# Kernel tuning notes

Measured on AMD Instinct MI355X. Metric: run time of the kernel, lower is better.

The kernel has to match this reference:

```python
import jax, jax.numpy as jnp
import numpy as np

T, B, L, CTX, H = 512, 512, 16, 64, 128
STATE_DIM, SHOT, PID, DATA = 32, 12, 35, 23


def setup_inputs() -> dict:
    key = jax.random.key(0)
    ks = jax.random.split(key, 64)
    k = iter(ks)
    def rn(shape, s=0.1):
        return (jax.random.normal(next(k), shape) * s).astype(jnp.float32)
    xs = jax.random.normal(next(k), (T, B, DATA), jnp.float32)
    xs = xs.at[:, :, 12].set(jax.random.randint(next(k), (T, B), 0, SHOT).astype(jnp.float32))
    xs = xs.at[:, :, 17].set(jax.random.randint(next(k), (T, B), 0, PID).astype(jnp.float32))
    xs = xs.at[:, :, 20].set(jax.random.randint(next(k), (T, B), 0, SHOT).astype(jnp.float32))
    return dict(
        total_xs=jnp.zeros((1,), jnp.float32),
        xs=xs,
        ts=jnp.linspace(0.0, 2.0, T).astype(jnp.float32),
        noise_std=jnp.asarray(0.1, jnp.float32),
        z0_noise=jax.random.normal(next(k), (B, L), jnp.float32),
        bm_noise=jax.random.normal(next(k), (T - 1, B, L), jnp.float32),
        shot_emb=rn((SHOT, 8)), player_emb=rn((PID, 8)),
        gru_wih=rn((3 * H, STATE_DIM)), gru_whh=rn((3 * H, H)),
        gru_bih=rn((3 * H,)), gru_bhh=rn((3 * H,)),
        enc_w=rn((CTX, H)), enc_b=rn((CTX,)),
        qz0_w=rn((2 * L, CTX)), qz0_b=rn((2 * L,)),
        f_w1=rn((H, L + CTX)), f_b1=rn((H,)), f_w2=rn((H, H)), f_b2=rn((H,)),
        f_w3=rn((L, H)), f_b3=rn((L,)),
        h_w1=rn((H, L)), h_b1=rn((H,)), h_w2=rn((H, H)), h_b2=rn((H,)),
        h_w3=rn((L, H)), h_b3=rn((L,)),
        g_w1=rn((L, H)), g_b1=rn((L, H)), g_w2=rn((L, H)), g_b2=rn((L,)),
        proj_w=rn((STATE_DIM, L)), proj_b=rn((STATE_DIM,)),
        pz0_mean=jnp.zeros((1, L), jnp.float32), pz0_logstd=jnp.zeros((1, L), jnp.float32),
        act_w=rn((128, L)), act_b=rn((128,)),
        act_land_w=rn((2, 128)), act_shot_w=rn((SHOT, 128)), act_move_w=rn((2, 128)),
    )


def _forward(xs, noise_std, shot_emb, player_emb, gru_wih, gru_whh, gru_bih, gru_bhh,
             enc_w, enc_b, qz0_w, qz0_b,
             f_w1, f_b1, f_w2, f_b2, f_w3, f_b3,
             h_w1, h_b1, h_w2, h_b2, h_w3, h_b3,
             g_w1, g_b1, g_w2, g_b2,
             proj_w, proj_b, pz0_mean, pz0_logstd,
             act_w, act_b, act_land_w, act_shot_w, act_move_w,
             ts, z0_noise, bm_noise):
    # --- SDE_embed_and_transform: replace shot/player id cols with embeddings ---
    state = xs[:, :, :18]
    shot_ids = state[:, :, 12].astype(jnp.int32)
    pid_ids = state[:, :, 17].astype(jnp.int32)
    state_t = jnp.concatenate([state[:, :, :12], shot_emb[shot_ids],
                               state[:, :, 13:17], player_emb[pid_ids]], axis=-1)  # (T,B,32)
    xs_t = jnp.concatenate([state_t, xs[:, :, 18:]], axis=-1)  # (T,B,37)
    # --- Encoder: GRU over time-reversed states, linear head, flip back ---
    def gru_step(h, xt):
        gi = xt @ gru_wih.T + gru_bih
        gh = h @ gru_whh.T + gru_bhh
        ir, iz, inn = jnp.split(gi, 3, axis=-1)
        hr, hz, hn = jnp.split(gh, 3, axis=-1)
        r = jax.nn.sigmoid(ir + hr)
        zg = jax.nn.sigmoid(iz + hz)
        n = jnp.tanh(inn + r * hn)
        hnew = (1.0 - zg) * n + zg * h
        return hnew, hnew
    h0 = jnp.zeros((xs.shape[1], gru_whh.shape[1]), xs.dtype)
    _, hs = jax.lax.scan(gru_step, h0, state_t[::-1])
    ctx = (hs @ enc_w.T + enc_b)[::-1]  # (T,B,CTX)
    # --- posterior z0 ---
    qm, qls = jnp.split(ctx[0] @ qz0_w.T + qz0_b, 2, axis=1)
    z0 = qm + jnp.exp(qls) * z0_noise
    # --- Euler-Maruyama with logqp; searchsorted(right) -> ctx[min(i+1,T-1)] = ctx[i+1] ---
    dts = ts[1:] - ts[:-1]  # (T-1,)
    dW = jnp.sqrt(dts)[:, None, None] * bm_noise
    ctx_steps = ctx[1:]
    def mlp3(x, w1, b1, w2, b2, w3, b3):
        h1 = jax.nn.softplus(x @ w1.T + b1)
        h2 = jax.nn.softplus(h1 @ w2.T + b2)
        return h2 @ w3.T + b3
    def g_diag(y):  # (B,L): per-latent-dim scalar nets, batched over L
        hg = jax.nn.softplus(y[:, :, None] * g_w1[None] + g_b1[None])  # (B,L,H)
        return jax.nn.sigmoid(jnp.einsum('blh,lh->bl', hg, g_w2) + g_b2)
    def sde_step(z, inp):
        c, dw, dt = inp
        f_val = mlp3(jnp.concatenate([z, c], axis=1), f_w1, f_b1, f_w2, f_b2, f_w3, f_b3)
        h_val = mlp3(z, h_w1, h_b1, h_w2, h_b2, h_w3, h_b3)
        g_val = g_diag(z)
        u = (f_val - h_val) / g_val
        logr = 0.5 * jnp.sum(u * u, axis=1) * dt
        z_new = z + f_val * dt + g_val * dw
        return z_new, (z_new, logr)
    _, (z_tail, log_ratio) = jax.lax.scan(sde_step, z0, (ctx_steps, dW, dts))
    zs = jnp.concatenate([z0[None], z_tail], axis=0)  # (T,B,L)
    _xs = zs @ proj_w.T + proj_b  # (T,B,32)
    # --- action model losses ---
    a = jax.nn.relu(zs @ act_w.T + act_b)
    land = (a @ act_land_w.T).reshape(-1, 2)
    shot_logits = (a @ act_shot_w.T).reshape(-1, act_shot_w.shape[0])
    move = (a @ act_move_w.T).reshape(-1, 2)
    true_actions = xs_t[:, :, -5:]
    true_land = true_actions[:, :, :2].reshape(-1, 2)
    true_move = true_actions[:, :, 3:].reshape(-1, 2)
    true_shot = true_actions[:, :, 2].astype(jnp.int32).reshape(-1)
    land_loss = jnp.mean((land - true_land) ** 2)
    move_loss = jnp.mean((move - true_move) ** 2)
    logp = jax.nn.log_softmax(shot_logits, axis=-1)
    picked = jnp.take_along_axis(logp, true_shot[:, None], axis=1)[:, 0]
    mask = (true_shot != 0).astype(logp.dtype)  # CrossEntropy ignore_index=0
    shot_loss = -jnp.sum(picked * mask) / jnp.maximum(jnp.sum(mask), 1.0)
    # --- reconstruction log-likelihood ---
    xs_state = xs_t[:, :, :STATE_DIM]
    LOG2PI = 1.8378770664093453
    log_pxs = jnp.mean(jnp.sum(
        -0.5 * ((xs_state - _xs) / noise_std) ** 2 - jnp.log(noise_std) - 0.5 * LOG2PI,
        axis=(0, 2)))
    # --- KL(q(z0) || p(z0)) ---
    var_q = jnp.exp(2.0 * qls)
    var_p = jnp.exp(2.0 * pz0_logstd)
    kl = pz0_logstd - qls + (var_q + (qm - pz0_mean) ** 2) / (2.0 * var_p) - 0.5
    logqp0 = jnp.mean(jnp.sum(kl, axis=1))
    logqp_path = jnp.mean(jnp.sum(log_ratio, axis=0))
    return log_pxs, logqp0 + logqp_path + land_loss + shot_loss + move_loss


def reference(total_xs, xs, ts, noise_std, z0_noise, bm_noise, shot_emb, player_emb,
              gru_wih, gru_whh, gru_bih, gru_bhh, enc_w, enc_b, qz0_w, qz0_b,
              f_w1, f_b1, f_w2, f_b2, f_w3, f_b3, h_w1, h_b1, h_w2, h_b2, h_w3, h_b3,
              g_w1, g_b1, g_w2, g_b2, proj_w, proj_b, pz0_mean, pz0_logstd,
              act_w, act_b, act_land_w, act_shot_w, act_move_w):
    return _forward(xs, noise_std, shot_emb, player_emb, gru_wih, gru_whh, gru_bih, gru_bhh,
                    enc_w, enc_b, qz0_w, qz0_b,
                    f_w1, f_b1, f_w2, f_b2, f_w3, f_b3,
                    h_w1, h_b1, h_w2, h_b2, h_w3, h_b3,
                    g_w1, g_b1, g_w2, g_b2,
                    proj_w, proj_b, pz0_mean, pz0_logstd,
                    act_w, act_b, act_land_w, act_shot_w, act_move_w,
                    ts, z0_noise, bm_noise)
```

## Files before the change

### kernel.cpp

```cpp
#include <hip/hip_runtime.h>
#include <cstdint>

typedef _Float16 f16;
typedef _Float16 f16x2 __attribute__((ext_vector_type(2)));

#define T_STEPS 512
#define B_SZ 512
#define LOG2PI 1.8378770664093453f

__device__ __forceinline__ void barrier_lds() {
  asm volatile("s_waitcnt lgkmcnt(0)" ::: "memory");
  __builtin_amdgcn_s_barrier();
  asm volatile("" ::: "memory");
}

__device__ __forceinline__ uint32_t packh2(float a, float b) {
  f16x2 v; v[0] = (f16)a; v[1] = (f16)b;
  return __builtin_bit_cast(uint32_t, v);
}

__device__ __forceinline__ float fdot2(uint32_t a, uint32_t b, float c) {
#if defined(__AMDGCN__) && __has_builtin(__builtin_amdgcn_fdot2)
  return __builtin_amdgcn_fdot2(__builtin_bit_cast(f16x2, a),
                                __builtin_bit_cast(f16x2, b), c, false);
#else
  f16x2 x = __builtin_bit_cast(f16x2, a), y = __builtin_bit_cast(f16x2, b);
  return c + (float)x[0] * (float)y[0] + (float)x[1] * (float)y[1];
#endif
}

#define DOT4(acc, w0, w1, w2, w3, v)                                     \
  do {                                                                   \
    acc = fdot2((w0), (v).x, acc); acc = fdot2((w1), (v).y, acc);        \
    acc = fdot2((w2), (v).z, acc); acc = fdot2((w3), (v).w, acc);        \
  } while (0)

__device__ __forceinline__ float sigmoidf_(float x) {
  return 1.0f / (1.0f + __expf(-x));
}
__device__ __forceinline__ float tanhf_(float x) {
  float ax = fabsf(x);
  float t = __expf(-2.0f * ax);
  float r = (1.0f - t) / (1.0f + t);
  return copysignf(r, x);
}
__device__ __forceinline__ float softplusf_(float x) {
  return fmaxf(x, 0.0f) + __logf(1.0f + __expf(-fabsf(x)));
}

__global__ __launch_bounds__(256) void k_embed(
    const float* __restrict__ xs, const float* __restrict__ shot_emb,
    const float* __restrict__ player_emb, f16* __restrict__ state_t,
    float* __restrict__ accums) {
  if (blockIdx.x == 0 && threadIdx.x < 16) accums[threadIdx.x] = 0.0f;
  size_t idx = (size_t)blockIdx.x * 256 + threadIdx.x;
  const float* xp = xs + idx * 23;
  f16* op = state_t + idx * 32;
  int sid = (int)xp[12];
  int pid = (int)xp[17];
#pragma unroll
  for (int i = 0; i < 12; ++i) op[i] = (f16)xp[i];
  const float* se = shot_emb + sid * 8;
#pragma unroll
  for (int i = 0; i < 8; ++i) op[12 + i] = (f16)se[i];
#pragma unroll
  for (int i = 0; i < 4; ++i) op[20 + i] = (f16)xp[13 + i];
  const float* pe = player_emb + pid * 8;
#pragma unroll
  for (int i = 0; i < 8; ++i) op[24 + i] = (f16)pe[i];
}

__global__ __launch_bounds__(256) void k_gtab(
    const float* __restrict__ gw1, const float* __restrict__ gb1,
    const float* __restrict__ gw2, const float* __restrict__ gb2,
    float* __restrict__ g_tab) {
  int gid = blockIdx.x * 256 + threadIdx.x;
  int l = gid >> 16, yi = gid & 0xffff;
  f16 hy = __builtin_bit_cast(f16, (unsigned short)yi);
  float y = (float)hy;
  const float* w1 = gw1 + l * 128;
  const float* b1 = gb1 + l * 128;
  const float* w2 = gw2 + l * 128;
  float a0 = 0.f, a1 = 0.f;
#pragma unroll 8
  for (int h = 0; h < 128; h += 2) {
    a0 = fmaf(softplusf_(fmaf(y, w1[h], b1[h])), w2[h], a0);
    a1 = fmaf(softplusf_(fmaf(y, w1[h + 1], b1[h + 1])), w2[h + 1], a1);
  }
  g_tab[gid] = sigmoidf_(a0 + a1 + gb2[l]);
}

__global__ __launch_bounds__(256, 2) void k_gru(
    const f16* __restrict__ state_t, const float* __restrict__ wih,
    const float* __restrict__ whh, const float* __restrict__ bih,
    const float* __restrict__ bhh, const float* __restrict__ enc_w,
    const float* __restrict__ enc_b, const float* __restrict__ qz0_w,
    const float* __restrict__ qz0_b, const float* __restrict__ z0_noise,
    const float* __restrict__ pz0_mean, const float* __restrict__ pz0_logstd,
    f16* __restrict__ ctx, float* __restrict__ z0_out,
    float* __restrict__ accums) {
  __shared__ uint32_t s_x[16];
  __shared__ uint32_t s_h[64];
  __shared__ float s_gates[128 * 4];
  __shared__ float s_encp[64 * 2];
  __shared__ float s_ctx0[64];
  __shared__ float s_q[32];

  const int tid = threadIdx.x;
  const int bg = blockIdx.x;
  const int r = tid >> 1, hh = tid & 1;
  const int ec = r & 63, eks = r >> 6;
  const uint32_t* stu = (const uint32_t*)state_t;

  uint32_t wR[32], wZ[32], wN[32];
  uint32_t wRx[8], wZx[8], wNx[8];
  uint32_t wE[16];
  {
    const float* w0 = whh + (size_t)(0 * 128 + r) * 128 + hh * 64;
    const float* w1 = whh + (size_t)(1 * 128 + r) * 128 + hh * 64;
    const float* w2 = whh + (size_t)(2 * 128 + r) * 128 + hh * 64;
#pragma unroll
    for (int i = 0; i < 32; ++i) {
      wR[i] = packh2(w0[2 * i], w0[2 * i + 1]);
      wZ[i] = packh2(w1[2 * i], w1[2 * i + 1]);
      wN[i] = packh2(w2[2 * i], w2[2 * i + 1]);
    }
    const float* x0 = wih + (size_t)(0 * 128 + r) * 32 + hh * 16;
    const float* x1 = wih + (size_t)(1 * 128 + r) * 32 + hh * 16;
    const float* x2 = wih + (size_t)(2 * 128 + r) * 32 + hh * 16;
#pragma unroll
    for (int i = 0; i < 8; ++i) {
      wRx[i] = packh2(x0[2 * i], x0[2 * i + 1]);
      wZx[i] = packh2(x1[2 * i], x1[2 * i + 1]);
      wNx[i] = packh2(x2[2 * i], x2[2 * i + 1]);
    }
    const float* we = enc_w + (size_t)ec * 128 + eks * 64 + hh * 32;
#pragma unroll
    for (int i = 0; i < 16; ++i) wE[i] = packh2(we[2 * i], we[2 * i + 1]);
  }
  const float bR = bih[r] + bhh[r];
  const float bZ = bih[128 + r] + bhh[128 + r];
  const float bNi = bih[256 + r];
  const float bNh = bhh[256 + r];
  float encbr = 0.f;
  if (tid >= 128 && tid < 192) encbr = enc_b[tid - 128];

  float h_old = 0.0f;
  if (tid < 64) s_h[tid] = 0u;
  if (tid < 4)
    *(uint4*)&s_x[tid * 4] =
        *(const uint4*)(stu + ((size_t)(T_STEPS - 1) * B_SZ + bg) * 16 + tid * 4);
  __syncthreads();

  for (int t = T_STEPS - 1; t >= 0; --t) {
    uint4 xpref = make_uint4(0, 0, 0, 0);
    if (tid >= 252 && t > 0)
      xpref = *(const uint4*)(stu +
                              ((size_t)(t - 1) * B_SZ + bg) * 16 + (tid - 252) * 4);
    {
      const uint4* xq = (const uint4*)&s_x[hh * 8];
      uint4 xv0 = xq[0], xv1 = xq[1];
      const uint4* hq = (const uint4*)&s_h[hh * 32];
      float aR = 0.f, aZ = 0.f, aNi = 0.f, aNh = 0.f;
      DOT4(aR, wRx[0], wRx[1], wRx[2], wRx[3], xv0);
      DOT4(aR, wRx[4], wRx[5], wRx[6], wRx[7], xv1);
      DOT4(aZ, wZx[0], wZx[1], wZx[2], wZx[3], xv0);
      DOT4(aZ, wZx[4], wZx[5], wZx[6], wZx[7], xv1);
      DOT4(aNi, wNx[0], wNx[1], wNx[2], wNx[3], xv0);
      DOT4(aNi, wNx[4], wNx[5], wNx[6], wNx[7], xv1);
#pragma unroll
      for (int j = 0; j < 8; ++j) {
        uint4 hv = hq[j];
        DOT4(aR, wR[4 * j], wR[4 * j + 1], wR[4 * j + 2], wR[4 * j + 3], hv);
        DOT4(aZ, wZ[4 * j], wZ[4 * j + 1], wZ[4 * j + 2], wZ[4 * j + 3], hv);
        DOT4(aNh, wN[4 * j], wN[4 * j + 1], wN[4 * j + 2], wN[4 * j + 3], hv);
      }
      aR += __shfl_xor(aR, 1);
      aZ += __shfl_xor(aZ, 1);
      aNi += __shfl_xor(aNi, 1);
      aNh += __shfl_xor(aNh, 1);
      if (hh == 0) {
        s_gates[r * 4 + 0] = aR + bR;
        s_gates[r * 4 + 2] = aNi + bNi;
      } else {
        s_gates[r * 4 + 1] = aZ + bZ;
        s_gates[r * 4 + 3] = aNh + bNh;
      }
      if (t < T_STEPS - 1) {
        const uint4* eq = (const uint4*)&s_h[eks * 32 + hh * 16];
        float aE = 0.f;
#pragma unroll
        for (int j = 0; j < 4; ++j) {
          uint4 ev = eq[j];
          DOT4(aE, wE[4 * j], wE[4 * j + 1], wE[4 * j + 2], wE[4 * j + 3], ev);
        }
        aE += __shfl_xor(aE, 1);
        if (hh == 0) s_encp[ec * 2 + eks] = aE;
      }
    }
    barrier_lds();
    if (tid < 128) {
      const float4 gt = *(const float4*)&s_gates[tid * 4];
      float rr = sigmoidf_(gt.x), zg = sigmoidf_(gt.y);
      float n = tanhf_(gt.z + rr * gt.w);
      float hnew = (1.0f - zg) * n + zg * h_old;
      h_old = hnew;
      ((f16*)&s_h[0])[tid] = (f16)hnew;
    } else if (tid < 192) {
      int c = tid - 128;
      if (t < T_STEPS - 1) {
        float v = s_encp[c * 2] + s_encp[c * 2 + 1] + encbr;
        ctx[((size_t)(t + 1) * B_SZ + bg) * 64 + c] = (f16)v;
      }
    }
    if (tid >= 252 && t > 0) *(uint4*)&s_x[(tid - 252) * 4] = xpref;
    barrier_lds();
  }

  {
    const uint4* eq = (const uint4*)&s_h[eks * 32 + hh * 16];
    float aE = 0.f;
#pragma unroll
    for (int j = 0; j < 4; ++j) {
      uint4 ev = eq[j];
      DOT4(aE, wE[4 * j], wE[4 * j + 1], wE[4 * j + 2], wE[4 * j + 3], ev);
    }
    aE += __shfl_xor(aE, 1);
    if (hh == 0) s_encp[ec * 2 + eks] = aE;
  }
  __syncthreads();
  if (tid < 64) {
    float v = s_encp[tid * 2] + s_encp[tid * 2 + 1] + enc_b[tid];
    ctx[(size_t)bg * 64 + tid] = (f16)v;
    s_ctx0[tid] = v;
  }
  __syncthreads();
  if (tid < 32) {
    float acc = qz0_b[tid];
#pragma unroll 8
    for (int k = 0; k < 64; ++k) acc += qz0_w[tid * 64 + k] * s_ctx0[k];
    s_q[tid] = acc;
  }
  __syncthreads();
  if (tid < 16) {
    float qm = s_q[tid], qls = s_q[16 + tid];
    float z0v = qm + __expf(qls) * z0_noise[bg * 16 + tid];
    z0_out[bg * 16 + tid] = z0v;
    float pm = pz0_mean[tid], pls = pz0_logstd[tid];
    float var_q = __expf(2.0f * qls);
    float var_p = __expf(2.0f * pls);
    float dm = qm - pm;
    float kl = pls - qls + (var_q + dm * dm) / (2.0f * var_p) - 0.5f;
    atomicAdd(&accums[5], kl);
  }
}

__global__ __launch_bounds__(256, 2) void k_sde(
    const f16* __restrict__ ctx, const float* __restrict__ z0_in,
    const float* __restrict__ ts, const float* __restrict__ bm_noise,
    const float* __restrict__ fw1, const float* __restrict__ fb1,
    const float* __restrict__ fw2, const float* __restrict__ fb2,
    const float* __restrict__ fw3, const float* __restrict__ fb3,
    const float* __restrict__ hw1, const float* __restrict__ hb1,
    const float* __restrict__ hw2, const float* __restrict__ hb2,
    const float* __restrict__ hw3, const float* __restrict__ hb3,
    const float* __restrict__ g_tab,
    f16* __restrict__ zs, float* __restrict__ accums) {
  __shared__ uint32_t s_x2[40];
  __shared__ uint32_t s_h1[2][64];
  __shared__ uint32_t s_h2[2][64];
  __shared__ float s_dts[T_STEPS];

  const int tid = threadIdx.x;
  const int bg = blockIdx.x;
  const uint4* ctx4 = (const uint4*)ctx;

  const int r1 = tid >> 1, hh = tid & 1;
  const int mlp2 = tid >> 7, u2 = tid & 127;
  const int l3 = (tid >> 3) & 15;
  const int mlp3 = (tid >> 2) & 1;
  const int kq = tid & 3;
  const bool p3act = (tid < 128);
  const bool zlane = p3act && ((tid & 7) == 0);
  const bool stg = (tid >= 128 && tid < 136);

  uint32_t uw1f[20], uw1h[4], wP2[64], wP3[16];
  float bf1r, bh1r, bias2r, fb3r = 0.f, hb3r = 0.f;
  {
    const float* w = fw1 + (size_t)r1 * 80 + hh * 40;
#pragma unroll
    for (int i = 0; i < 20; ++i) uw1f[i] = packh2(w[2 * i], w[2 * i + 1]);
    bf1r = fb1[r1];
  }
  {
    const float* w = hw1 + (size_t)r1 * 16 + hh * 8;
#pragma unroll
    for (int i = 0; i < 4; ++i) uw1h[i] = packh2(w[2 * i], w[2 * i + 1]);
    bh1r = hb1[r1];
  }
  {
    const float* w = (mlp2 ? hw2 : fw2) + (size_t)u2 * 128;
#pragma unroll
    for (int i = 0; i < 64; ++i) wP2[i] = packh2(w[2 * i], w[2 * i + 1]);
    bias2r = (mlp2 ? hb2 : fb2)[u2];
  }
  if (p3act) {
    const float* w = (mlp3 ? hw3 : fw3) + (size_t)l3 * 128 + kq * 32;
#pragma unroll
    for (int i = 0; i < 16; ++i) wP3[i] = packh2(w[2 * i], w[2 * i + 1]);
    fb3r = fb3[l3];
    hb3r = hb3[l3];
  }
  for (int i = tid; i < T_STEPS - 1; i += 256) s_dts[i] = ts[i + 1] - ts[i];

  float zreg = 0.f, bmc = 0.f, path_acc = 0.f;
  uint4 cpref = make_uint4(0, 0, 0, 0);
  if (zlane) {
    zreg = z0_in[bg * 16 + l3];
    ((f16*)&s_x2[0])[l3] = (f16)zreg;
    zs[(size_t)bg * 16 + l3] = (f16)zreg;
    bmc = bm_noise[(size_t)bg * 16 + l3];
  }
  if (stg) {
    int q = tid - 128;
    uint4 v = ctx4[((size_t)1 * B_SZ + bg) * 8 + q];
    *(uint4*)&s_x2[8 + q * 4] = v;
  }
  __syncthreads();

  for (int t = 0; t < T_STEPS - 1; ++t) {
    float bmn = 0.f, gvp = 0.f;
    if (zlane) {
      unsigned short zb = __builtin_bit_cast(unsigned short, (f16)zreg);
      gvp = g_tab[l3 * 65536 + (int)zb];
      if (t < T_STEPS - 2)
        bmn = bm_noise[((size_t)(t + 1) * B_SZ + bg) * 16 + l3];
    }
    if (stg && t <= T_STEPS - 3)
      cpref = ctx4[((size_t)(t + 2) * B_SZ + bg) * 8 + (tid - 128)];

    {
      const uint4* xq = (const uint4*)&s_x2[0];
      const int base = hh * 5;
      float a0 = 0.f, a1 = 0.f;
      {
        uint4 v0 = xq[base + 0], v1 = xq[base + 1];
        DOT4(a0, uw1f[0], uw1f[1], uw1f[2], uw1f[3], v0);
        DOT4(a1, uw1f[4], uw1f[5], uw1f[6], uw1f[7], v1);
        uint4 v2 = xq[base + 2], v3 = xq[base + 3];
        DOT4(a0, uw1f[8], uw1f[9], uw1f[10], uw1f[11], v2);
        DOT4(a1, uw1f[12], uw1f[13], uw1f[14], uw1f[15], v3);
        uint4 v4 = xq[base + 4];
        DOT4(a0, uw1f[16], uw1f[17], uw1f[18], uw1f[19], v4);
      }
      float af = a0 + a1;
      uint4 vz = xq[hh];
      float ah = 0.f;
      DOT4(ah, uw1h[0], uw1h[1], uw1h[2], uw1h[3], vz);
      float ff = af + __shfl_xor(af, 1);
      float fh = ah + __shfl_xor(ah, 1);
      if (hh == 0)
        ((f16*)&s_h1[0][0])[r1] = (f16)softplusf_(ff + bf1r);
      else
        ((f16*)&s_h1[1][0])[r1] = (f16)softplusf_(fh + bh1r);
    }
    barrier_lds();
    {
      const uint4* hq = (const uint4*)&s_h1[mlp2][0];
      float a0 = 0.f, a1 = 0.f;
#pragma unroll
      for (int j = 0; j < 16; j += 2) {
        uint4 v0 = hq[j], v1 = hq[j + 1];
        DOT4(a0, wP2[4 * j], wP2[4 * j + 1], wP2[4 * j + 2], wP2[4 * j + 3], v0);
        DOT4(a1, wP2[4 * j + 4], wP2[4 * j + 5], wP2[4 * j + 6], wP2[4 * j + 7], v1);
      }
      ((f16*)&s_h2[mlp2][0])[u2] = (f16)softplusf_(a0 + a1 + bias2r);
    }
    barrier_lds();
    if (p3act) {
      const uint4* hq = (const uint4*)&s_h2[mlp3][kq * 16];
      float a0 = 0.f, a1 = 0.f;
#pragma unroll
      for (int j = 0; j < 4; j += 2) {
        uint4 v0 = hq[j], v1 = hq[j + 1];
        DOT4(a0, wP3[4 * j], wP3[4 * j + 1], wP3[4 * j + 2], wP3[4 * j + 3], v0);
        DOT4(a1, wP3[4 * j + 4], wP3[4 * j + 5], wP3[4 * j + 6], wP3[4 * j + 7], v1);
      }
      float a = a0 + a1;
      float s1 = a + __shfl_xor(a, 1);
      float s2 = s1 + __shfl_xor(s1, 2);
      float other = __shfl_xor(s2, 4);
      if ((tid & 7) == 0) {
        float fv = s2 + fb3r;
        float hv = other + hb3r;
        float gv = gvp;
        float dt = s_dts[t];
        float u_ = (fv - hv) / gv;
        float ls = u_ * u_;
        ls += __shfl_xor(ls, 8);
        ls += __shfl_xor(ls, 16);
        ls += __shfl_xor(ls, 32);
        if ((tid & 63) == 0) path_acc += 0.5f * ls * dt;
        float dw = sqrtf(dt) * bmc;
        float zn = zreg + fv * dt + gv * dw;
        zreg = zn;
        ((f16*)&s_x2[0])[l3] = (f16)zn;
        zs[((size_t)(t + 1) * B_SZ + bg) * 16 + l3] = (f16)zn;
        bmc = bmn;
      }
    } else if (stg && t <= T_STEPS - 3) {
      *(uint4*)&s_x2[8 + (tid - 128) * 4] = cpref;
    }
    barrier_lds();
  }
  if (tid == 0 || tid == 64) atomicAdd(&accums[6], path_acc);
}

__global__ __launch_bounds__(256) void k_dec(
    const f16* __restrict__ zs, const f16* __restrict__ state_t,
    const float* __restrict__ xs, const float* __restrict__ proj_w,
    const float* __restrict__ proj_b, const float* __restrict__ act_w,
    const float* __restrict__ act_b, const float* __restrict__ land_w,
    const float* __restrict__ shot_w, const float* __restrict__ move_w,
    float* __restrict__ accums) {
  __shared__ uint32_t s_proj[8 * 32];
  __shared__ uint32_t s_act[8 * 128];
  __shared__ uint32_t s_head[128 * 8];
  __shared__ float s_pb[32], s_ab[128];
  __shared__ float s_red[4 * 5];

  const int tid = threadIdx.x;
  for (int id = tid; id < 8 * 32; id += 256) {
    int kp = id & 7, n = id >> 3;
    s_proj[kp * 32 + n] = packh2(proj_w[n * 16 + 2 * kp], proj_w[n * 16 + 2 * kp + 1]);
  }
  for (int id = tid; id < 8 * 128; id += 256) {
    int kp = id & 7, n = id >> 3;
    s_act[kp * 128 + n] = packh2(act_w[n * 16 + 2 * kp], act_w[n * 16 + 2 * kp + 1]);
  }
  for (int id = tid; id < 128 * 8; id += 256) {
    int j = id >> 3, p = id & 7;
    int h0 = 2 * p, h1 = 2 * p + 1;
    float w0 = (h0 < 2) ? land_w[h0 * 128 + j]
                        : (h0 < 14 ? shot_w[(h0 - 2) * 128 + j]
                                   : move_w[(h0 - 14) * 128 + j]);
    float w1 = (h1 < 2) ? land_w[h1 * 128 + j]
                        : (h1 < 14 ? shot_w[(h1 - 2) * 128 + j]
                                   : move_w[(h1 - 14) * 128 + j]);
    s_head[j * 8 + p] = packh2(w0, w1);
  }
  if (tid < 32) s_pb[tid] = proj_b[tid];
  if (tid < 128) s_ab[tid] = act_b[tid];
  __syncthreads();

  size_t idx = (size_t)blockIdx.x * 256 + tid;
  uint32_t z2[8];
  const uint32_t* zp = (const uint32_t*)(zs + idx * 16);
#pragma unroll
  for (int i = 0; i < 8; ++i) z2[i] = zp[i];
  uint32_t stv[16];
  const uint32_t* stp = (const uint32_t*)(state_t + idx * 32);
#pragma unroll
  for (int i = 0; i < 16; ++i) stv[i] = stp[i];

  float sqsum = 0.0f;
#pragma unroll 4
  for (int i = 0; i < 32; ++i) {
    float acc = s_pb[i];
#pragma unroll
    for (int kp = 0; kp < 8; ++kp) acc = fdot2(s_proj[kp * 32 + i], z2[kp], acc);
    f16x2 sv = __builtin_bit_cast(f16x2, stv[i >> 1]);
    float d = (float)sv[i & 1] - acc;
    sqsum += d * d;
  }

  float hd[16];
#pragma unroll
  for (int i = 0; i < 16; ++i) hd[i] = 0.0f;
#pragma unroll 2
  for (int j = 0; j < 128; ++j) {
    float a = s_ab[j];
#pragma unroll
    for (int kp = 0; kp < 8; ++kp) a = fdot2(s_act[kp * 128 + j], z2[kp], a);
    a = fmaxf(a, 0.0f);
#pragma unroll
    for (int p = 0; p < 8; ++p) {
      f16x2 w = __builtin_bit_cast(f16x2, s_head[j * 8 + p]);
      hd[2 * p] += (float)w[0] * a;
      hd[2 * p + 1] += (float)w[1] * a;
    }
  }
  const float* xp = xs + idx * 23;
  float dl0 = hd[0] - xp[18], dl1 = hd[1] - xp[19];
  float land = dl0 * dl0 + dl1 * dl1;
  float dm0 = hd[14] - xp[21], dm1 = hd[15] - xp[22];
  float move = dm0 * dm0 + dm1 * dm1;
  int sid = (int)xp[20];
  float m = hd[2];
#pragma unroll
  for (int s = 1; s < 12; ++s) m = fmaxf(m, hd[2 + s]);
  float sume = 0.0f;
#pragma unroll
  for (int s = 0; s < 12; ++s) sume += __expf(hd[2 + s] - m);
  float lse = m + __logf(sume);
  float pl = 0.0f;
#pragma unroll
  for (int s = 0; s < 12; ++s)
    if (s == sid) pl = hd[2 + s];
  float picked = 0.0f, cnt = 0.0f;
  if (sid != 0) {
    picked = pl - lse;
    cnt = 1.0f;
  }
  float vals[5] = {sqsum, land, move, picked, cnt};
#pragma unroll
  for (int v = 0; v < 5; ++v) {
    float x = vals[v];
    for (int off = 1; off < 64; off <<= 1) x += __shfl_xor(x, off);
    vals[v] = x;
  }
  int lane = tid & 63, wv = tid >> 6;
  if (lane == 0) {
#pragma unroll
    for (int v = 0; v < 5; ++v) s_red[wv * 5 + v] = vals[v];
  }
  __syncthreads();
  if (tid == 0) {
#pragma unroll
    for (int v = 0; v < 5; ++v) {
      float s = s_red[v] + s_red[5 + v] + s_red[10 + v] + s_red[15 + v];
      atomicAdd(&accums[v], s);
    }
  }
}

__global__ void k_fin(const float* __restrict__ accums,
                      const float* __restrict__ noise_std,
                      float* __restrict__ out) {
  if (threadIdx.x == 0 && blockIdx.x == 0) {
    float sd = noise_std[0];
    float log_pxs = -0.5f * accums[0] / (sd * sd * (float)B_SZ) -
                    (float)T_STEPS * 32.0f * (logf(sd) + 0.5f * LOG2PI);
    float land = accums[1] / (float)(T_STEPS * B_SZ * 2);
    float move = accums[2] / (float)(T_STEPS * B_SZ * 2);
    float shot = -accums[3] / fmaxf(accums[4], 1.0f);
    float out1 = accums[5] / (float)B_SZ + accums[6] / (float)B_SZ + land + shot + move;
    out[0] = log_pxs;
    out[1] = out1;
  }
}

extern "C" void kernel_launch(void* const* d_in, const int* in_sizes, int n_in,
                              void* d_out, int out_size, void* d_ws,
                              size_t ws_size, hipStream_t stream) {
  const float* xs = (const float*)d_in[1];
  const float* ts = (const float*)d_in[2];
  const float* noise_std = (const float*)d_in[3];
  const float* z0_noise = (const float*)d_in[4];
  const float* bm_noise = (const float*)d_in[5];
  const float* shot_emb = (const float*)d_in[6];
  const float* player_emb = (const float*)d_in[7];
  const float* gru_wih = (const float*)d_in[8];
  const float* gru_whh = (const float*)d_in[9];
  const float* gru_bih = (const float*)d_in[10];
  const float* gru_bhh = (const float*)d_in[11];
  const float* enc_w = (const float*)d_in[12];
  const float* enc_b = (const float*)d_in[13];
  const float* qz0_w = (const float*)d_in[14];
  const float* qz0_b = (const float*)d_in[15];
  const float* f_w1 = (const float*)d_in[16];
  const float* f_b1 = (const float*)d_in[17];
  const float* f_w2 = (const float*)d_in[18];
  const float* f_b2 = (const float*)d_in[19];
  const float* f_w3 = (const float*)d_in[20];
  const float* f_b3 = (const float*)d_in[21];
  const float* h_w1 = (const float*)d_in[22];
  const float* h_b1 = (const float*)d_in[23];
  const float* h_w2 = (const float*)d_in[24];
  const float* h_b2 = (const float*)d_in[25];
  const float* h_w3 = (const float*)d_in[26];
  const float* h_b3 = (const float*)d_in[27];
  const float* g_w1 = (const float*)d_in[28];
  const float* g_b1 = (const float*)d_in[29];
  const float* g_w2 = (const float*)d_in[30];
  const float* g_b2 = (const float*)d_in[31];
  const float* proj_w = (const float*)d_in[32];
  const float* proj_b = (const float*)d_in[33];
  const float* pz0_mean = (const float*)d_in[34];
  const float* pz0_logstd = (const float*)d_in[35];
  const float* act_w = (const float*)d_in[36];
  const float* act_b = (const float*)d_in[37];
  const float* act_land_w = (const float*)d_in[38];
  const float* act_shot_w = (const float*)d_in[39];
  const float* act_move_w = (const float*)d_in[40];

  char* ws = (char*)d_ws;
  float* accums = (float*)ws;
  f16* state_t = (f16*)(ws + 256);
  f16* ctx = (f16*)(ws + 256 + 16777216);
  float* z0b = (float*)(ws + 256 + 16777216 + 33554432);
  f16* zs = (f16*)(ws + 256 + 16777216 + 33554432 + 32768);
  float* g_tab = (float*)(ws + 256 + 16777216 + 33554432 + 32768 + 8388608);

  k_embed<<<1024, 256, 0, stream>>>(xs, shot_emb, player_emb, state_t, accums);
  k_gtab<<<4096, 256, 0, stream>>>(g_w1, g_b1, g_w2, g_b2, g_tab);
  k_gru<<<512, 256, 0, stream>>>(state_t, gru_wih, gru_whh, gru_bih, gru_bhh,
                                 enc_w, enc_b, qz0_w, qz0_b, z0_noise, pz0_mean,
                                 pz0_logstd, ctx, z0b, accums);
  k_sde<<<512, 256, 0, stream>>>(ctx, z0b, ts, bm_noise, f_w1, f_b1, f_w2, f_b2,
                                 f_w3, f_b3, h_w1, h_b1, h_w2, h_b2, h_w3, h_b3,
                                 g_tab, zs, accums);
  k_dec<<<1024, 256, 0, stream>>>(zs, state_t, xs, proj_w, proj_b, act_w, act_b,
                                  act_land_w, act_shot_w, act_move_w, accums);
  k_fin<<<1, 64, 0, stream>>>(accums, noise_std, (float*)d_out);
}
```

Baseline: 1.628 ms.

## Double-buffer GRU hidden state to drop one barrier per timestep

After: 1.616 ms. About the same (-0.7%).

```diff
diff --git a/kernel.cpp b/kernel.cpp
--- a/kernel.cpp
+++ b/kernel.cpp
@@ -99,17 +99,15 @@
     const float* __restrict__ pz0_mean, const float* __restrict__ pz0_logstd,
     f16* __restrict__ ctx, float* __restrict__ z0_out,
     float* __restrict__ accums) {
-  __shared__ uint32_t s_x[16];
-  __shared__ uint32_t s_h[64];
-  __shared__ float s_gates[128 * 4];
-  __shared__ float s_encp[64 * 2];
+  __shared__ uint32_t s_x[2][16];
+  __shared__ uint32_t s_h[2][64];
   __shared__ float s_ctx0[64];
   __shared__ float s_q[32];
 
   const int tid = threadIdx.x;
   const int bg = blockIdx.x;
   const int r = tid >> 1, hh = tid & 1;
-  const int ec = r & 63, eks = r >> 6;
+  const int ec = tid >> 2, eks = (tid >> 1) & 1;
   const uint32_t* stu = (const uint32_t*)state_t;
 
   uint32_t wR[32], wZ[32], wN[32];
@@ -142,25 +140,31 @@
   const float bZ = bih[128 + r] + bhh[128 + r];
   const float bNi = bih[256 + r];
   const float bNh = bhh[256 + r];
-  float encbr = 0.f;
-  if (tid >= 128 && tid < 192) encbr = enc_b[tid - 128];
+  const float encbc = enc_b[ec];
 
   float h_old = 0.0f;
-  if (tid < 64) s_h[tid] = 0u;
+  if (tid < 64) s_h[0][tid] = 0u;
   if (tid < 4)
-    *(uint4*)&s_x[tid * 4] =
+    *(uint4*)&s_x[0][tid * 4] =
         *(const uint4*)(stu + ((size_t)(T_STEPS - 1) * B_SZ + bg) * 16 + tid * 4);
+  uint4 xpref = make_uint4(0, 0, 0, 0);
+  if (tid >= 252)
+    xpref = *(const uint4*)(stu +
+                            ((size_t)(T_STEPS - 2) * B_SZ + bg) * 16 + (tid - 252) * 4);
   __syncthreads();
 
   for (int t = T_STEPS - 1; t >= 0; --t) {
-    uint4 xpref = make_uint4(0, 0, 0, 0);
-    if (tid >= 252 && t > 0)
-      xpref = *(const uint4*)(stu +
-                              ((size_t)(t - 1) * B_SZ + bg) * 16 + (tid - 252) * 4);
+    const int rb = (t + 1) & 1, wb = t & 1;
+    if (tid >= 252) {
+      if (t > 0) *(uint4*)&s_x[wb][(tid - 252) * 4] = xpref;
+      if (t > 1)
+        xpref = *(const uint4*)(stu +
+                                ((size_t)(t - 2) * B_SZ + bg) * 16 + (tid - 252) * 4);
+    }
     {
-      const uint4* xq = (const uint4*)&s_x[hh * 8];
+      const uint4* xq = (const uint4*)&s_x[rb][hh * 8];
       uint4 xv0 = xq[0], xv1 = xq[1];
-      const uint4* hq = (const uint4*)&s_h[hh * 32];
+      const uint4* hq = (const uint4*)&s_h[rb][hh * 32];
       float aR = 0.f, aZ = 0.f, aNi = 0.f, aNh = 0.f;
       DOT4(aR, wRx[0], wRx[1], wRx[2], wRx[3], xv0);
       DOT4(aR, wRx[4], wRx[5], wRx[6], wRx[7], xv1);
@@ -179,46 +183,31 @@
       aZ += __shfl_xor(aZ, 1);
       aNi += __shfl_xor(aNi, 1);
       aNh += __shfl_xor(aNh, 1);
-      if (hh == 0) {
-        s_gates[r * 4 + 0] = aR + bR;
-        s_gates[r * 4 + 2] = aNi + bNi;
-      } else {
-        s_gates[r * 4 + 1] = aZ + bZ;
-        s_gates[r * 4 + 3] = aNh + bNh;
-      }
-      if (t < T_STEPS - 1) {
-        const uint4* eq = (const uint4*)&s_h[eks * 32 + hh * 16];
-        float aE = 0.f;
-#pragma unroll
-        for (int j = 0; j < 4; ++j) {
-          uint4 ev = eq[j];
-          DOT4(aE, wE[4 * j], wE[4 * j + 1], wE[4 * j + 2], wE[4 * j + 3], ev);
-        }
-        aE += __shfl_xor(aE, 1);
-        if (hh == 0) s_encp[ec * 2 + eks] = aE;
-      }
-    }
-    barrier_lds();
-    if (tid < 128) {
-      const float4 gt = *(const float4*)&s_gates[tid * 4];
-      float rr = sigmoidf_(gt.x), zg = sigmoidf_(gt.y);
-      float n = tanhf_(gt.z + rr * gt.w);
+      float rr = sigmoidf_(aR + bR);
+      float zg = sigmoidf_(aZ + bZ);
+      float n = tanhf_(aNi + bNi + rr * (aNh + bNh));
       float hnew = (1.0f - zg) * n + zg * h_old;
       h_old = hnew;
-      ((f16*)&s_h[0])[tid] = (f16)hnew;
-    } else if (tid < 192) {
-      int c = tid - 128;
-      if (t < T_STEPS - 1) {
-        float v = s_encp[c * 2] + s_encp[c * 2 + 1] + encbr;
-        ctx[((size_t)(t + 1) * B_SZ + bg) * 64 + c] = (f16)v;
+      if (hh == 0) ((f16*)&s_h[wb][0])[r] = (f16)hnew;
+    }
+    if (t < T_STEPS - 1) {
+      const uint4* eq = (const uint4*)&s_h[rb][eks * 32 + hh * 16];
+      float aE = 0.f;
+#pragma unroll
+      for (int j = 0; j < 4; ++j) {
+        uint4 ev = eq[j];
+        DOT4(aE, wE[4 * j], wE[4 * j + 1], wE[4 * j + 2], wE[4 * j + 3], ev);
       }
-    }
-    if (tid >= 252 && t > 0) *(uint4*)&s_x[(tid - 252) * 4] = xpref;
+      aE += __shfl_xor(aE, 1);
+      aE += __shfl_xor(aE, 2);
+      if ((tid & 3) == 0)
+        ctx[((size_t)(t + 1) * B_SZ + bg) * 64 + ec] = (f16)(aE + encbc);
+    }
     barrier_lds();
   }
 
   {
-    const uint4* eq = (const uint4*)&s_h[eks * 32 + hh * 16];
+    const uint4* eq = (const uint4*)&s_h[0][eks * 32 + hh * 16];
     float aE = 0.f;
 #pragma unroll
     for (int j = 0; j < 4; ++j) {
@@ -226,13 +215,12 @@
       DOT4(aE, wE[4 * j], wE[4 * j + 1], wE[4 * j + 2], wE[4 * j + 3], ev);
     }
     aE += __shfl_xor(aE, 1);
-    if (hh == 0) s_encp[ec * 2 + eks] = aE;
-  }
-  __syncthreads();
-  if (tid < 64) {
-    float v = s_encp[tid * 2] + s_encp[tid * 2 + 1] + enc_b[tid];
-    ctx[(size_t)bg * 64 + tid] = (f16)v;
-    s_ctx0[tid] = v;
+    aE += __shfl_xor(aE, 2);
+    if ((tid & 3) == 0) {
+      float v = aE + encbc;
+      ctx[(size_t)bg * 64 + ec] = (f16)v;
+      s_ctx0[ec] = v;
+    }
   }
   __syncthreads();
   if (tid < 32) {
```
